# Optimization experiments

Measured on AMD Instinct MI355X. Metric: run time of the kernel, lower is better.

The kernel has to match this reference:

```python
import jax, jax.numpy as jnp
import numpy as np

ALPHA = 1.0
LN_EPS = 1e-5


def b2bsqrt(x):
    # sign(x) * (sqrt(alpha + |x|) - sqrt(alpha)), alpha = 1.0
    return jnp.sign(x) * (jnp.sqrt(ALPHA + jnp.abs(x)) - jnp.sqrt(ALPHA))


def setup_inputs() -> dict:
    key = jax.random.key(0)
    ks = jax.random.split(key, 4)
    B, T, F, H, C = 512, 100, 1024, 1024, 10
    sW = 1.0 / np.sqrt(F)
    sU = 1.0 / np.sqrt(H)
    return {
        "x": jax.random.normal(ks[0], (B, T, F), dtype=jnp.float32),
        "W": jax.random.normal(ks[1], (4, F, H), dtype=jnp.float32) * sW,  # gates [i, f, o, c]
        "U": jax.random.normal(ks[2], (4, H, H), dtype=jnp.float32) * sU,
        "b": jnp.zeros((4, H), dtype=jnp.float32),
        "ln_g": jnp.ones((H,), dtype=jnp.float32),
        "ln_b": jnp.zeros((H,), dtype=jnp.float32),
        "fc_w": jax.random.normal(ks[3], (H, C), dtype=jnp.float32) * sU,
        "fc_b": jnp.zeros((C,), dtype=jnp.float32),
    }


def _lstm_b2bsqrt(x, W, U, b):
    # x: (B, T, F) -> h_seq: (B, T, H). Gate order in W/U/b: [i, f, o, c].
    B, T, F = x.shape
    H = W.shape[-1]
    # Precompute input projections for all steps: (T, 4, B, H)
    xz = jnp.einsum('btf,gfh->tgbh', x, W) + b[None, :, None, :]

    def step(carry, xz_t):
        h, c = carry
        z = xz_t + jnp.einsum('bh,ghk->gbk', h, U)  # (4, B, H)
        i = jax.nn.sigmoid(z[0])
        f = jax.nn.sigmoid(z[1])
        o = jax.nn.sigmoid(z[2])
        c_tilda = b2bsqrt(z[3])
        c = f * c + i * c_tilda
        h = o * b2bsqrt(c)
        return (h, c), h

    h0 = jnp.zeros((B, H), dtype=x.dtype)
    c0 = jnp.zeros((B, H), dtype=x.dtype)
    _, h_seq = jax.lax.scan(step, (h0, c0), xz)  # (T, B, H)
    return jnp.transpose(h_seq, (1, 0, 2))  # (B, T, H)


def reference(x, W, U, b, ln_g, ln_b, fc_w, fc_b):
    h = _lstm_b2bsqrt(x, W, U, b)  # (B, T, H)
    # features_to_logits: per-step LayerNorm then Linear.
    # NOTE: in the original code, activation_logit's output is discarded
    # (y_class = fc_logits(y) uses the layernormed y), reproduced faithfully.
    mu = jnp.mean(h, axis=-1, keepdims=True)
    var = jnp.mean(jnp.square(h - mu), axis=-1, keepdims=True)
    y = (h - mu) * jax.lax.rsqrt(var + LN_EPS) * ln_g + ln_b
    logits = jnp.einsum('bth,hc->btc', y, fc_w) + fc_b  # (B, T, num_classes)
    return logits
```

## Files before the change

kernel.cpp:

```cpp
#include <hip/hip_runtime.h>
#include <stdint.h>

typedef __bf16 bf16;
typedef __bf16 bf16x4 __attribute__((ext_vector_type(4)));
typedef __bf16 bf16x8 __attribute__((ext_vector_type(8)));
typedef float f32x4 __attribute__((ext_vector_type(4)));
typedef unsigned int u32x2 __attribute__((ext_vector_type(2)));

#define MFMA16x16x32(A, B, C) __builtin_amdgcn_mfma_f32_16x16x32_bf16((A), (B), (C), 0, 0, 0)

#define B_ 512
#define T_ 100
#define F_ 1024
#define H_ 1024
#define TC_ 10

__device__ __forceinline__ float sigmoid_f(float x) { return 1.0f / (1.0f + __expf(-x)); }
__device__ __forceinline__ float b2bsqrt_f(float x) {
  float s = sqrtf(1.0f + fabsf(x)) - 1.0f;
  return x >= 0.0f ? s : -s;
}

__device__ __forceinline__ void glds16(const void* g, void* l) {
  __builtin_amdgcn_global_load_lds((const __attribute__((address_space(1))) void*)g,
                                   (__attribute__((address_space(3))) void*)l, 16, 0, 0);
}

__global__ __launch_bounds__(256) void zero_init(bf16* __restrict__ h0,
                                                 float* __restrict__ c0,
                                                 unsigned* __restrict__ bars, int n) {
  int i = blockIdx.x * blockDim.x + threadIdx.x;
  if (i < n) { h0[i] = (bf16)0.0f; c0[i] = 0.0f; }
  if (i < 10 * 1024) bars[i] = 0u;
}

__global__ __launch_bounds__(256) void tr_kernel(const float* __restrict__ src,
                                                 bf16* __restrict__ dst) {
  __shared__ float tile[32][33];
  int g = blockIdx.z;
  int c0 = blockIdx.x * 32;
  int r0 = blockIdx.y * 32;
  const float* s = src + (size_t)g * 1024 * 1024;
  bf16* d = dst + (size_t)g * 1024 * 1024;
  int tx = threadIdx.x & 31, ty = threadIdx.x >> 5;
  #pragma unroll
  for (int i = 0; i < 32; i += 8)
    tile[ty + i][tx] = s[(size_t)(r0 + ty + i) * 1024 + c0 + tx];
  __syncthreads();
  #pragma unroll
  for (int i = 0; i < 32; i += 8)
    d[(size_t)(c0 + ty + i) * 1024 + r0 + tx] = (bf16)tile[tx][ty + i];
}

__global__ __launch_bounds__(256) void convx(const float* __restrict__ x,
                                             bf16* __restrict__ xbf, int t0) {
  int lr = blockIdx.x * 4 + (threadIdx.x >> 6);
  int lane = threadIdx.x & 63;
  unsigned b = (unsigned)lr / 10u;
  unsigned tt = (unsigned)lr - b * 10u;
  const float* src = x + (size_t)(b * 100u + (unsigned)t0 + tt) * 1024;
  bf16* dst = xbf + (size_t)lr * 1024;
  #pragma unroll
  for (int j = 0; j < 4; ++j) {
    f32x4 f = *(const f32x4*)(src + (j * 64 + lane) * 4);
    bf16x4 o;
    o[0] = (bf16)f[0]; o[1] = (bf16)f[1]; o[2] = (bf16)f[2]; o[3] = (bf16)f[3];
    *(bf16x4*)(dst + (j * 64 + lane) * 4) = o;
  }
}

__global__ __launch_bounds__(256) void prep_fc(const float* __restrict__ lng,
                                               const float* __restrict__ lnb,
                                               const float* __restrict__ fcw,
                                               const float* __restrict__ fcb,
                                               bf16* __restrict__ Bt,
                                               float* __restrict__ SA) {
  __shared__ float red[2][256];
  int c = blockIdx.x;
  int tid = threadIdx.x;
  float pS = 0.f, pA = 0.f;
  #pragma unroll
  for (int j = 0; j < 4; ++j) {
    int h = j * 256 + tid;
    float v;
    if (c < 10) {
      float wv = fcw[h * 10 + c];
      v = lng[h] * wv;
      pS += v;
      pA += lnb[h] * wv;
    } else {
      v = (c == 10) ? 1.0f : 0.0f;
    }
    Bt[c * 1024 + h] = (bf16)v;
  }
  if (c < 10) {
    red[0][tid] = pS; red[1][tid] = pA;
    __syncthreads();
    for (int s = 128; s > 0; s >>= 1) {
      if (tid < s) { red[0][tid] += red[0][tid + s]; red[1][tid] += red[1][tid + s]; }
      __syncthreads();
    }
    if (tid == 0) { SA[c] = red[0][0]; SA[16 + c] = red[1][0] + fcb[c]; }
  }
}

__global__ __launch_bounds__(256) void gemm_xz(const bf16* __restrict__ X,
                                               const bf16* __restrict__ Wt,
                                               bf16* __restrict__ XZc) {
  __shared__ bf16 sA[128 * 32];
  __shared__ bf16 sB[128 * 32];
  const int tid = threadIdx.x;
  const int lane = tid & 63;
  const int w = tid >> 6;
  const int l16 = lane & 15;
  const int quad = lane >> 4;
  const int m0 = blockIdx.y * 128;
  const int n0 = blockIdx.x * 128;
  const int wm = (w >> 1) * 64;
  const int wn = (w & 1) * 64;
  const int rA = lane >> 2;
  const int gch = (lane & 3) ^ (rA & 3);

  f32x4 acc[4][4] = {};

  for (int kk = 0; kk < 1024; kk += 32) {
    #pragma unroll
    for (int j = 0; j < 2; ++j) {
      int r0 = (w * 2 + j) * 16;
      int r = r0 + rA;
      glds16(X + (size_t)(m0 + r) * 1024 + kk + gch * 8, sA + r0 * 32);
      glds16(Wt + (size_t)(n0 + r) * 1024 + kk + gch * 8, sB + r0 * 32);
    }
    __syncthreads();
    bf16x8 aF[4], bF[4];
    const int slot = quad ^ (l16 & 3);
    #pragma unroll
    for (int mt = 0; mt < 4; ++mt)
      aF[mt] = *(const bf16x8*)(sA + (wm + mt * 16 + l16) * 32 + slot * 8);
    #pragma unroll
    for (int nt = 0; nt < 4; ++nt)
      bF[nt] = *(const bf16x8*)(sB + (wn + nt * 16 + l16) * 32 + slot * 8);
    #pragma unroll
    for (int mt = 0; mt < 4; ++mt)
      #pragma unroll
      for (int nt = 0; nt < 4; ++nt)
        acc[mt][nt] = MFMA16x16x32(aF[mt], bF[nt], acc[mt][nt]);
    __syncthreads();
  }

  #pragma unroll
  for (int mt = 0; mt < 4; ++mt) {
    #pragma unroll
    for (int r = 0; r < 4; ++r) {
      unsigned lr = (unsigned)(m0 + wm + mt * 16 + quad * 4 + r);
      unsigned b = lr / 10u;
      unsigned tt = lr - b * 10u;
      #pragma unroll
      for (int nt = 0; nt < 4; ++nt) {
        int n = n0 + wn + nt * 16 + l16;
        int g = n >> 10;
        int hh = n & 1023;
        XZc[((size_t)(tt * 4 + g) * B_ + b) * H_ + hh] = (bf16)acc[mt][nt][r];
      }
    }
  }
}

__global__ __launch_bounds__(512, 1) void step_persist(
    int t0,
    const bf16* __restrict__ XZc,
    const bf16* __restrict__ Ut,
    const float* __restrict__ bias,
    bf16* __restrict__ hseq,
    float* __restrict__ cst,
    unsigned* __restrict__ bar) {
  __shared__ __align__(16) unsigned char smem[131072];
  bf16* sA = (bf16*)smem;
  float* sZf = (float*)smem;

  const int tid = threadIdx.x;
  const int lane = tid & 63;
  const int w = tid >> 6;
  const int gate = w & 3;
  const int hf = w >> 2;
  const int l16 = lane & 15;
  const int quad = lane >> 4;
  const int bid = blockIdx.x;
  const int bm0 = (bid & 7) * 64;
  const int hn0 = (bid >> 3) * 32;
  unsigned* const grp = &bar[(bid & 7) * 64];

  bf16x8 bfr[2][16];
  #pragma unroll
  for (int nt = 0; nt < 2; ++nt) {
    const bf16* up = Ut + (size_t)((gate << 10) + hn0 + nt * 16 + l16) * 1024 + hf * 128 + quad * 8;
    #pragma unroll
    for (int t = 0; t < 4; ++t)
      #pragma unroll
      for (int kh = 0; kh < 4; ++kh)
        bfr[nt][t * 4 + kh] = *(const bf16x8*)(up + t * 256 + kh * 32);
  }

  const int rr = tid >> 3;
  const int cc = (tid & 7) * 4;
  const int gb = bm0 + rr;
  const int gh = hn0 + cc;
  f32x4 creg = *(const f32x4*)(cst + (size_t)gb * H_ + gh);
  f32x4 bs[4];
  #pragma unroll
  for (int g = 0; g < 4; ++g) bs[g] = *(const f32x4*)(bias + g * H_ + gh);

  const int srow = w * 8 + (lane >> 5);
  const int lch = lane & 31;

  bf16x4 xzv[4];
  #pragma unroll
  for (int g = 0; g < 4; ++g)
    xzv[g] = *(const bf16x4*)(XZc + ((size_t)(0 * 4 + g) * B_ + gb) * H_ + gh);

  unsigned btarget = 0;

  for (int tt = 0; tt < TC_; ++tt) {
    const bf16* hp = hseq + (size_t)(t0 + tt) * B_ * H_;
    bf16* hnx = hseq + (size_t)(t0 + tt + 1) * B_ * H_;

    #pragma unroll
    for (int t = 0; t < 4; ++t)
      #pragma unroll
      for (int i = 0; i < 4; ++i) {
        const int r = bm0 + srow + i * 2;
        glds16(hp + (size_t)r * 1024 + (size_t)(t * 32 + (lch ^ (r & 15))) * 8,
               smem + t * 32768 + (size_t)(w * 8 + i * 2) * 512);
      }

    f32x4 acc[4][2] = {};

    #pragma unroll
    for (int t = 0; t < 4; ++t) {
      if (t == 0)      asm volatile("s_waitcnt vmcnt(12)" ::: "memory");
      else if (t == 1) asm volatile("s_waitcnt vmcnt(8)" ::: "memory");
      else if (t == 2) asm volatile("s_waitcnt vmcnt(4)" ::: "memory");
      else             asm volatile("s_waitcnt vmcnt(0)" ::: "memory");
      __builtin_amdgcn_sched_barrier(0);
      __builtin_amdgcn_s_barrier();
      __builtin_amdgcn_sched_barrier(0);
      #pragma unroll
      for (int kh = 0; kh < 4; ++kh) {
        const int S = hf * 16 + kh * 4 + quad;
        const int slot = S ^ l16;
        bf16x8 aF[4];
        #pragma unroll
        for (int mt = 0; mt < 4; ++mt)
          aF[mt] = *(const bf16x8*)(sA + (size_t)t * 16384 + (mt * 16 + l16) * 256 + slot * 8);
        #pragma unroll
        for (int mt = 0; mt < 4; ++mt) {
          acc[mt][0] = MFMA16x16x32(aF[mt], bfr[0][t * 4 + kh], acc[mt][0]);
          acc[mt][1] = MFMA16x16x32(aF[mt], bfr[1][t * 4 + kh], acc[mt][1]);
        }
      }
      __builtin_amdgcn_sched_barrier(0);
    }

    #pragma unroll
    for (int mt = 0; mt < 4; ++mt)
      #pragma unroll
      for (int nt = 0; nt < 2; ++nt)
        #pragma unroll
        for (int r = 0; r < 4; ++r)
          sZf[w * 2304 + (mt * 16 + quad * 4 + r) * 36 + nt * 16 + l16] = acc[mt][nt][r];
    __syncthreads();

    f32x4 z[4];
    #pragma unroll
    for (int g = 0; g < 4; ++g) {
      f32x4 za = *(const f32x4*)(sZf + g * 2304 + rr * 36 + cc);
      f32x4 zb = *(const f32x4*)(sZf + (g + 4) * 2304 + rr * 36 + cc);
      z[g] = za + zb;
    }
    bf16x4 hb;
    #pragma unroll
    for (int jj = 0; jj < 4; ++jj) {
      float I  = sigmoid_f(z[0][jj] + (float)xzv[0][jj] + bs[0][jj]);
      float Fg = sigmoid_f(z[1][jj] + (float)xzv[1][jj] + bs[1][jj]);
      float O  = sigmoid_f(z[2][jj] + (float)xzv[2][jj] + bs[2][jj]);
      float Ct = b2bsqrt_f(z[3][jj] + (float)xzv[3][jj] + bs[3][jj]);
      float c2 = Fg * creg[jj] + I * Ct;
      creg[jj] = c2;
      hb[jj] = (bf16)(O * b2bsqrt_f(c2));
    }
    {
      u32x2 hbu = __builtin_bit_cast(u32x2, hb);
      bf16* ha = hnx + (size_t)gb * H_ + gh;
      asm volatile("global_store_dwordx2 %0, %1, off sc0 sc1" :: "v"(ha), "v"(hbu) : "memory");
    }

    if (tt < TC_ - 1) {
      #pragma unroll
      for (int g = 0; g < 4; ++g)
        xzv[g] = *(const bf16x4*)(XZc + ((size_t)((tt + 1) * 4 + g) * B_ + gb) * H_ + gh);

      btarget += 32u;
      __syncthreads();
      if (tid == 0) {
        atomicAdd(grp, 1u);
        unsigned spins = 0;
        while (__hip_atomic_load(grp, __ATOMIC_RELAXED, __HIP_MEMORY_SCOPE_AGENT)
               < btarget) {
          __builtin_amdgcn_s_sleep(1);
          if (++spins > (1u << 22)) break;
        }
        __builtin_amdgcn_fence(__ATOMIC_ACQUIRE, "agent");
      }
      __syncthreads();
    }
  }

  *(f32x4*)(cst + (size_t)gb * H_ + gh) = creg;
}

__global__ __launch_bounds__(256) void ln_fc_kernel(
    const bf16* __restrict__ hseq1, const bf16* __restrict__ Bt,
    const float* __restrict__ SA, float* __restrict__ out) {
  __shared__ bf16 sA[64 * 64];
  __shared__ bf16 sBt[16 * 1040];
  __shared__ float sLg[4][16 * 17];
  __shared__ float sSq[4][16];
  const int tid = threadIdx.x;
  const int lane = tid & 63;
  const int w = tid >> 6;
  const int l16 = lane & 15;
  const int quad = lane >> 4;
  const int m0 = blockIdx.x * 64;
  const int rL = lane >> 3;
  const int gch = (lane & 7) ^ rL;

  #pragma unroll
  for (int i = 0; i < 8; ++i) {
    int ch = tid + i * 256;
    int n = ch >> 7, k8 = ch & 127;
    *(bf16x8*)(sBt + n * 1040 + k8 * 8) = *(const bf16x8*)(Bt + n * 1024 + k8 * 8);
  }

  f32x4 acc = {};
  float sq = 0.f;

  for (int kk = 0; kk < 1024; kk += 64) {
    #pragma unroll
    for (int j = 0; j < 2; ++j) {
      int r0 = (w * 2 + j) * 8;
      int r = r0 + rL;
      glds16(hseq1 + (size_t)(m0 + r) * 1024 + kk + gch * 8, sA + r0 * 64);
    }
    __syncthreads();
    #pragma unroll
    for (int kh = 0; kh < 2; ++kh) {
      const int slot = (kh * 4 + quad) ^ (l16 & 7);
      bf16x8 aF = *(const bf16x8*)(sA + (w * 16 + l16) * 64 + slot * 8);
      bf16x8 bF = *(const bf16x8*)(sBt + l16 * 1040 + kk + kh * 32 + quad * 8);
      acc = MFMA16x16x32(aF, bF, acc);
      #pragma unroll
      for (int e = 0; e < 8; ++e) { float f = (float)aF[e]; sq += f * f; }
    }
    __syncthreads();
  }

  sq += __shfl_xor(sq, 16, 64);
  sq += __shfl_xor(sq, 32, 64);

  #pragma unroll
  for (int r = 0; r < 4; ++r)
    sLg[w][(quad * 4 + r) * 17 + l16] = acc[r];
  if (quad == 0) sSq[w][l16] = sq;
  __syncthreads();

  if (lane < 16) {
    int row = lane;
    float sum = sLg[w][row * 17 + 10];
    float ssq = sSq[w][row];
    float mu = sum * (1.0f / 1024.0f);
    float var = ssq * (1.0f / 1024.0f) - mu * mu;
    float rs = rsqrtf(var + 1e-5f);
    int rg = m0 + w * 16 + row;
    int t = rg >> 9, b = rg & 511;
    float* op = out + ((size_t)b * 100 + t) * 10;
    #pragma unroll
    for (int c = 0; c < 10; ++c)
      op[c] = rs * (sLg[w][row * 17 + c] - mu * SA[c]) + SA[16 + c];
  }
}

extern "C" void kernel_launch(void* const* d_in, const int* in_sizes, int n_in,
                              void* d_out, int out_size, void* d_ws, size_t ws_size,
                              hipStream_t stream) {
  (void)in_sizes; (void)n_in; (void)out_size; (void)ws_size;
  const float* x    = (const float*)d_in[0];
  const float* W    = (const float*)d_in[1];
  const float* U    = (const float*)d_in[2];
  const float* bias = (const float*)d_in[3];
  const float* lng  = (const float*)d_in[4];
  const float* lnb  = (const float*)d_in[5];
  const float* fcw  = (const float*)d_in[6];
  const float* fcb  = (const float*)d_in[7];
  float* out = (float*)d_out;

  char* ws = (char*)d_ws;
  size_t off = 0;
  bf16* Wt   = (bf16*)(ws + off); off += (size_t)4 * F_ * H_ * 2;
  bf16* Ut   = (bf16*)(ws + off); off += (size_t)4 * H_ * H_ * 2;
  bf16* XZc  = (bf16*)(ws + off); off += (size_t)TC_ * 4 * B_ * H_ * 2;
  bf16* hseq = (bf16*)(ws + off); off += (size_t)(T_ + 1) * B_ * H_ * 2;
  float* cst = (float*)(ws + off); off += (size_t)B_ * H_ * 4;
  bf16* xbf  = (bf16*)(ws + off); off += (size_t)B_ * TC_ * F_ * 2;
  bf16* Bt   = (bf16*)(ws + off); off += (size_t)16 * H_ * 2;
  float* SA  = (float*)(ws + off); off += 32 * 4;
  unsigned* bars = (unsigned*)(ws + off); off += 10 * 1024 * 4;

  zero_init<<<(B_ * H_ + 255) / 256, 256, 0, stream>>>(hseq, cst, bars, B_ * H_);
  tr_kernel<<<dim3(32, 32, 4), 256, 0, stream>>>(W, Wt);
  tr_kernel<<<dim3(32, 32, 4), 256, 0, stream>>>(U, Ut);
  prep_fc<<<16, 256, 0, stream>>>(lng, lnb, fcw, fcb, Bt, SA);

  for (int chunk = 0; chunk < T_ / TC_; ++chunk) {
    int t0 = chunk * TC_;
    convx<<<(B_ * TC_) / 4, 256, 0, stream>>>(x, xbf, t0);
    gemm_xz<<<dim3(32, (B_ * TC_) / 128), 256, 0, stream>>>(xbf, Wt, XZc);
    step_persist<<<256, 512, 0, stream>>>(t0, XZc, Ut, bias, hseq, cst,
                                          bars + chunk * 1024);
  }

  ln_fc_kernel<<<(B_ * T_) / 64, 256, 0, stream>>>(hseq + (size_t)B_ * H_, Bt, SA, out);
}
```

Baseline: 1.803 ms.

## Replace chunked time loop with single full-sequence GEMM and persistent recurrence kernel

Drops the 10-chunk host loop. The input conversion and the input-projection GEMM now run once over all 100 timesteps, and a single persistent step kernel runs every timestep with the cell state held in registers. This removes repeated kernel launches, cross-launch cell-state save/restore, and small-GEMM inefficiency, at the cost of a much larger XZ workspace. It also removes the acquire fence after the grid barrier spin, which could allow stale hidden-state reads between timesteps.

```diff
diff --git a/kernel.cpp b/kernel.cpp
--- a/kernel.cpp
+++ b/kernel.cpp
@@ -13,7 +13,6 @@
 #define T_ 100
 #define F_ 1024
 #define H_ 1024
-#define TC_ 10
 
 __device__ __forceinline__ float sigmoid_f(float x) { return 1.0f / (1.0f + __expf(-x)); }
 __device__ __forceinline__ float b2bsqrt_f(float x) {
@@ -27,11 +26,10 @@
 }
 
 __global__ __launch_bounds__(256) void zero_init(bf16* __restrict__ h0,
-                                                 float* __restrict__ c0,
                                                  unsigned* __restrict__ bars, int n) {
   int i = blockIdx.x * blockDim.x + threadIdx.x;
-  if (i < n) { h0[i] = (bf16)0.0f; c0[i] = 0.0f; }
-  if (i < 10 * 1024) bars[i] = 0u;
+  if (i < n) h0[i] = (bf16)0.0f;
+  if (i < 512) bars[i] = 0u;
 }
 
 __global__ __launch_bounds__(256) void tr_kernel(const float* __restrict__ src,
@@ -52,21 +50,21 @@
     d[(size_t)(c0 + ty + i) * 1024 + r0 + tx] = (bf16)tile[tx][ty + i];
 }
 
-__global__ __launch_bounds__(256) void convx(const float* __restrict__ x,
-                                             bf16* __restrict__ xbf, int t0) {
-  int lr = blockIdx.x * 4 + (threadIdx.x >> 6);
-  int lane = threadIdx.x & 63;
-  unsigned b = (unsigned)lr / 10u;
-  unsigned tt = (unsigned)lr - b * 10u;
-  const float* src = x + (size_t)(b * 100u + (unsigned)t0 + tt) * 1024;
-  bf16* dst = xbf + (size_t)lr * 1024;
+__global__ __launch_bounds__(256) void convx_all(const float* __restrict__ x,
+                                                 bf16* __restrict__ xbf) {
+  size_t i = ((size_t)blockIdx.x * 256 + threadIdx.x) * 16;
+  bf16x8 o0, o1;
+  f32x4 f0 = *(const f32x4*)(x + i);
+  f32x4 f1 = *(const f32x4*)(x + i + 4);
+  f32x4 f2 = *(const f32x4*)(x + i + 8);
+  f32x4 f3 = *(const f32x4*)(x + i + 12);
   #pragma unroll
   for (int j = 0; j < 4; ++j) {
-    f32x4 f = *(const f32x4*)(src + (j * 64 + lane) * 4);
-    bf16x4 o;
-    o[0] = (bf16)f[0]; o[1] = (bf16)f[1]; o[2] = (bf16)f[2]; o[3] = (bf16)f[3];
-    *(bf16x4*)(dst + (j * 64 + lane) * 4) = o;
-  }
+    o0[j] = (bf16)f0[j]; o0[4 + j] = (bf16)f1[j];
+    o1[j] = (bf16)f2[j]; o1[4 + j] = (bf16)f3[j];
+  }
+  *(bf16x8*)(xbf + i) = o0;
+  *(bf16x8*)(xbf + i + 8) = o1;
 }
 
 __global__ __launch_bounds__(256) void prep_fc(const float* __restrict__ lng,
@@ -153,26 +151,24 @@
     #pragma unroll
     for (int r = 0; r < 4; ++r) {
       unsigned lr = (unsigned)(m0 + wm + mt * 16 + quad * 4 + r);
-      unsigned b = lr / 10u;
-      unsigned tt = lr - b * 10u;
+      unsigned b = lr / 100u;
+      unsigned t = lr - b * 100u;
       #pragma unroll
       for (int nt = 0; nt < 4; ++nt) {
         int n = n0 + wn + nt * 16 + l16;
         int g = n >> 10;
         int hh = n & 1023;
-        XZc[((size_t)(tt * 4 + g) * B_ + b) * H_ + hh] = (bf16)acc[mt][nt][r];
+        XZc[((size_t)(t * 4 + g) * B_ + b) * H_ + hh] = (bf16)acc[mt][nt][r];
       }
     }
   }
 }
 
 __global__ __launch_bounds__(512, 1) void step_persist(
-    int t0,
     const bf16* __restrict__ XZc,
     const bf16* __restrict__ Ut,
     const float* __restrict__ bias,
     bf16* __restrict__ hseq,
-    float* __restrict__ cst,
     unsigned* __restrict__ bar) {
   __shared__ __align__(16) unsigned char smem[131072];
   bf16* sA = (bf16*)smem;
@@ -205,7 +201,7 @@
   const int cc = (tid & 7) * 4;
   const int gb = bm0 + rr;
   const int gh = hn0 + cc;
-  f32x4 creg = *(const f32x4*)(cst + (size_t)gb * H_ + gh);
+  f32x4 creg = {0.f, 0.f, 0.f, 0.f};
   f32x4 bs[4];
   #pragma unroll
   for (int g = 0; g < 4; ++g) bs[g] = *(const f32x4*)(bias + g * H_ + gh);
@@ -220,9 +216,9 @@
 
   unsigned btarget = 0;
 
-  for (int tt = 0; tt < TC_; ++tt) {
-    const bf16* hp = hseq + (size_t)(t0 + tt) * B_ * H_;
-    bf16* hnx = hseq + (size_t)(t0 + tt + 1) * B_ * H_;
+  for (int tt = 0; tt < T_; ++tt) {
+    const bf16* hp = hseq + (size_t)tt * B_ * H_;
+    bf16* hnx = hseq + (size_t)(tt + 1) * B_ * H_;
 
     #pragma unroll
     for (int t = 0; t < 4; ++t)
@@ -294,7 +290,7 @@
       asm volatile("global_store_dwordx2 %0, %1, off sc0 sc1" :: "v"(ha), "v"(hbu) : "memory");
     }
 
-    if (tt < TC_ - 1) {
+    if (tt < T_ - 1) {
       #pragma unroll
       for (int g = 0; g < 4; ++g)
         xzv[g] = *(const bf16x4*)(XZc + ((size_t)((tt + 1) * 4 + g) * B_ + gb) * H_ + gh);
@@ -309,13 +305,10 @@
           __builtin_amdgcn_s_sleep(1);
           if (++spins > (1u << 22)) break;
         }
-        __builtin_amdgcn_fence(__ATOMIC_ACQUIRE, "agent");
       }
       __syncthreads();
     }
   }
-
-  *(f32x4*)(cst + (size_t)gb * H_ + gh) = creg;
 }
 
 __global__ __launch_bounds__(256) void ln_fc_kernel(
@@ -407,26 +400,21 @@
   size_t off = 0;
   bf16* Wt   = (bf16*)(ws + off); off += (size_t)4 * F_ * H_ * 2;
   bf16* Ut   = (bf16*)(ws + off); off += (size_t)4 * H_ * H_ * 2;
-  bf16* XZc  = (bf16*)(ws + off); off += (size_t)TC_ * 4 * B_ * H_ * 2;
+  bf16* XZc  = (bf16*)(ws + off); off += (size_t)T_ * 4 * B_ * H_ * 2;
   bf16* hseq = (bf16*)(ws + off); off += (size_t)(T_ + 1) * B_ * H_ * 2;
-  float* cst = (float*)(ws + off); off += (size_t)B_ * H_ * 4;
-  bf16* xbf  = (bf16*)(ws + off); off += (size_t)B_ * TC_ * F_ * 2;
+  bf16* xbf  = (bf16*)(ws + off); off += (size_t)B_ * T_ * F_ * 2;
   bf16* Bt   = (bf16*)(ws + off); off += (size_t)16 * H_ * 2;
   float* SA  = (float*)(ws + off); off += 32 * 4;
-  unsigned* bars = (unsigned*)(ws + off); off += 10 * 1024 * 4;
-
-  zero_init<<<(B_ * H_ + 255) / 256, 256, 0, stream>>>(hseq, cst, bars, B_ * H_);
+  unsigned* bars = (unsigned*)(ws + off); off += 512 * 4;
+
+  zero_init<<<(B_ * H_ + 255) / 256, 256, 0, stream>>>(hseq, bars, B_ * H_);
   tr_kernel<<<dim3(32, 32, 4), 256, 0, stream>>>(W, Wt);
   tr_kernel<<<dim3(32, 32, 4), 256, 0, stream>>>(U, Ut);
   prep_fc<<<16, 256, 0, stream>>>(lng, lnb, fcw, fcb, Bt, SA);
 
-  for (int chunk = 0; chunk < T_ / TC_; ++chunk) {
-    int t0 = chunk * TC_;
-    convx<<<(B_ * TC_) / 4, 256, 0, stream>>>(x, xbf, t0);
-    gemm_xz<<<dim3(32, (B_ * TC_) / 128), 256, 0, stream>>>(xbf, Wt, XZc);
-    step_persist<<<256, 512, 0, stream>>>(t0, XZc, Ut, bias, hseq, cst,
-                                          bars + chunk * 1024);
-  }
+  convx_all<<<(B_ * T_ * F_) / (256 * 16), 256, 0, stream>>>(x, xbf);
+  gemm_xz<<<dim3(32, (B_ * T_) / 128), 256, 0, stream>>>(xbf, Wt, XZc);
+  step_persist<<<256, 512, 0, stream>>>(XZc, Ut, bias, hseq, bars);
 
   ln_fc_kernel<<<(B_ * T_) / 64, 256, 0, stream>>>(hseq + (size_t)B_ * H_, Bt, SA, out);
 }
```

Result: faster. 1.601 ms (-11.2%).
